# Performance work log

Measured on AMD Instinct MI355X. Metric: run time of the kernel, lower is better.

Reference implementation:

```python
import jax, jax.numpy as jnp
import numpy as np

DIM = 192


def _conv1x1(x, w, b):
    # x: [B, C_in, H, W], w: [C_out, C_in], b: [C_out]
    return jnp.einsum('bchw,oc->bohw', x, w) + b[None, :, None, None]


def setup_inputs() -> dict:
    key = jax.random.key(0)
    ks = jax.random.split(key, 7)
    B, T, C, H, W = 4, 16, DIM, 56, 56
    scale = 1.0 / np.sqrt(2 * C)
    return {
        'video': jax.random.normal(ks[0], (B, T, C, H, W), dtype=jnp.float32),
        'w_z': jax.random.normal(ks[1], (C, 2 * C), dtype=jnp.float32) * scale,
        'b_z': jax.random.normal(ks[2], (C,), dtype=jnp.float32) * scale,
        'w_r': jax.random.normal(ks[3], (C, 2 * C), dtype=jnp.float32) * scale,
        'b_r': jax.random.normal(ks[4], (C,), dtype=jnp.float32) * scale,
        'w_h': jax.random.normal(ks[5], (C, 2 * C), dtype=jnp.float32) * scale,
        'b_h': jax.random.normal(ks[6], (C,), dtype=jnp.float32) * scale,
    }


def reference(video, w_z, b_z, w_r, b_r, w_h, b_h):
    # video: [B, T, C, H, W]
    h0 = jnp.zeros_like(video[:, 0])  # [B, C, H, W]

    def step(h, x):
        xh = jnp.concatenate([x, h], axis=1)  # [B, 2C, H, W]
        z = jax.nn.sigmoid(_conv1x1(xh, w_z, b_z))
        r = jax.nn.sigmoid(_conv1x1(xh, w_r, b_r))
        xrh = jnp.concatenate([x, r * h], axis=1)
        h_new = (1.0 - z) * h + z * jnp.tanh(_conv1x1(xrh, w_h, b_h))
        return h_new, h_new

    # scan over time axis
    _, out = jax.lax.scan(step, h0, jnp.moveaxis(video, 1, 0))
    return jnp.moveaxis(out, 0, 1)  # [B, T, C, H, W]
```

## Files before the change

kernel.cpp:

```cpp
#include <hip/hip_runtime.h>
#include <cstdint>
#include <cstddef>

typedef _Float16 f16;
typedef _Float16 half8 __attribute__((ext_vector_type(8)));
typedef _Float16 half4 __attribute__((ext_vector_type(4)));
typedef float f32x4 __attribute__((ext_vector_type(4)));
typedef unsigned int u32;
typedef u32 u32x4 __attribute__((ext_vector_type(4)));

constexpr int CDIM = 192, HW = 3136, NBAT = 4, TSTEPS = 16;
constexpr int MTOT = NBAT * HW;
constexpr int NSUB = MTOT / 16;

constexpr size_t OFF_WX = 0;
constexpr size_t SZ_WX  = (size_t)6*36*64*8*2;
constexpr size_t OFF_WHB = OFF_WX + SZ_WX;
constexpr size_t SZ_WHB  = (size_t)12*3*6*64*8*2;
constexpr size_t OFF_U  = OFF_WHB + SZ_WHB;
constexpr size_t SZ_U   = (size_t)16*NSUB*12*3*64*4*2;
constexpr size_t NEED   = OFF_U + SZ_U;

constexpr size_t FB_WZR = 0;
constexpr size_t FB_SZ_WZR = (size_t)384*384*2;
constexpr size_t FB_WH  = FB_WZR + FB_SZ_WZR;


__global__ void pack_w(const float* __restrict__ wz, const float* __restrict__ wr,
                       const float* __restrict__ wh, char* __restrict__ ws) {
    int idx = blockIdx.x * 256 + threadIdx.x;
    if (idx >= 221184) return;
    f16* dst;
    int lane, i, k, c, gate;
    if (idx < 110592) {
        i = idx & 7; lane = (idx >> 3) & 63;
        int ktnt = idx >> 9, kt = ktnt / 36, nt = ktnt % 36;
        int n576 = nt * 16 + (lane & 15);
        gate = n576 / 192; c = n576 % 192;
        k = kt * 32 + (lane >> 4) * 8 + i;
        dst = (f16*)(ws + OFF_WX) + idx;
    } else {
        int j = idx - 110592;
        i = j & 7; lane = (j >> 3) & 63;
        int a = j >> 9, kt = a % 6, b = a / 6;
        gate = b % 3; int nsl = b / 3;
        c = nsl * 16 + (lane & 15);
        k = 192 + kt * 32 + (lane >> 4) * 8 + i;
        dst = (f16*)(ws + OFF_WHB) + j;
    }
    const float* W = (gate == 0) ? wz : (gate == 1) ? wr : wh;
    *dst = (f16)W[c * 384 + k];
}

__global__ __launch_bounds__(512, 2) void xproj(
    const float* __restrict__ video, char* __restrict__ ws,
    const float* __restrict__ bz, const float* __restrict__ br,
    const float* __restrict__ bh) {
    __shared__ __align__(16) char AX[2][24576];
    const f16* WX = (const f16*)(ws + OFF_WX);
    f16* U = (f16*)(ws + OFF_U);
    const int tid = threadIdx.x, w = tid >> 6, lane = tid & 63;
    const int l15 = lane & 15, lg = lane >> 4;
    const int mt = blockIdx.x;
    const int bb = mt / 49, hw0 = (mt % 49) * 64;
    const int t0 = blockIdx.y * 2;
    const int mg = w >> 2, nw = w & 3;
    const int swsh = (lane & 7) << 4;
    const int slot = (l15 & 7) << 4;

#pragma unroll
    for (int p = 0; p < 2; ++p) {
        const float* vs = video + ((size_t)(bb * TSTEPS + t0 + p) * CDIM) * HW + hw0 + lane;
#pragma unroll
        for (int g = 0; g < 3; ++g) {
            half8 hv;
#pragma unroll
            for (int j = 0; j < 8; ++j)
                hv[j] = (f16)__builtin_nontemporal_load(vs + (size_t)(w * 24 + g * 8 + j) * HW);
            *(half8*)(AX[p] + lane * 384 + ((w * 48 + g * 16) ^ swsh)) = hv;
        }
    }
    float vb[9];
#pragma unroll
    for (int r = 0; r < 9; ++r) {
        int n576 = nw * 144 + r * 16 + l15;
        int gate = n576 / 192, c = n576 % 192;
        vb[r] = (gate == 0 ? bz : (gate == 1 ? br : bh))[c];
    }
    __syncthreads();

    f32x4 acc[4][9];
#pragma unroll
    for (int i = 0; i < 4; ++i)
#pragma unroll
        for (int r = 0; r < 9; ++r)
#pragma unroll
            for (int q = 0; q < 4; ++q) acc[i][r][q] = vb[r];

#pragma unroll
    for (int kt = 0; kt < 6; ++kt) {
        half8 a[4];
#pragma unroll
        for (int i = 0; i < 4; ++i)
            a[i] = *(const half8*)(AX[mg] + (i * 16 + l15) * 384 + ((kt * 64 + lg * 16) ^ slot));
#pragma unroll
        for (int r = 0; r < 9; ++r) {
            half8 bf = *(const half8*)(WX + ((size_t)(kt * 36 + nw * 9 + r) * 64 + lane) * 8);
#pragma unroll
            for (int i = 0; i < 4; ++i)
                acc[i][r] = __builtin_amdgcn_mfma_f32_16x16x32_f16(a[i], bf, acc[i][r], 0, 0, 0);
        }
    }
    const int t = t0 + mg;
#pragma unroll
    for (int r = 0; r < 9; ++r) {
        int nb = nw * 9 + r;
        int gate = nb / 12, nsl = nb % 12;
#pragma unroll
        for (int i = 0; i < 4; ++i) {
            half4 hq;
#pragma unroll
            for (int q = 0; q < 4; ++q) hq[q] = (f16)acc[i][r][q];
            int sub = mt * 4 + i;
            f16* up = U + (((size_t)t * NSUB + sub) * 36 + (size_t)nsl * 3 + gate) * 256
                        + (size_t)lane * 4;
            *(half4*)up = hq;
        }
    }
}

__global__ __launch_bounds__(768, 3) void recur(const char* __restrict__ ws,
                                                float* __restrict__ dout) {
    __shared__ __align__(16) char AH[6144], RH[6144];
    const f16* WHB = (const f16*)(ws + OFF_WHB);
    const f16* U = (const f16*)(ws + OFF_U);
    const int tid = threadIdx.x, wv = tid >> 6, lane = tid & 63;
    const int l15 = lane & 15, lg = lane >> 4;
    const int sub = blockIdx.x;
    const int bb = sub / 196, hw0 = (sub % 196) * 16;
    const int slot = (l15 & 7) << 4;
    const int col = wv * 16 + l15;

    half8 wz_[6], wr_[6], wh_[6];
    {
        const f16* base = WHB + (size_t)wv * 9216 + lane * 8;
#pragma unroll
        for (int kt = 0; kt < 6; ++kt) {
            wz_[kt] = *(const half8*)(base + (0 * 6 + kt) * 512);
            wr_[kt] = *(const half8*)(base + (1 * 6 + kt) * 512);
            wh_[kt] = *(const half8*)(base + (2 * 6 + kt) * 512);
        }
    }
    *(uint64_t*)(AH + tid * 8) = 0ull;
    __syncthreads();

    const f16* ub = U + ((size_t)sub * 36 + (size_t)wv * 3) * 256 + (size_t)lane * 4;
    constexpr size_t UT = (size_t)NSUB * 36 * 256;
    half4 uz = *(const half4*)(ub);
    half4 ur = *(const half4*)(ub + 256);
    half4 uh = *(const half4*)(ub + 512);

    float h_own[4] = {0.f, 0.f, 0.f, 0.f};
    const int cb = (2 * col);
    float* ob = dout + ((size_t)(bb * TSTEPS) * CDIM + col) * HW + hw0 + lg * 4;

#pragma unroll 1
    for (int t = 0; t < TSTEPS; ++t) {
        f32x4 az = {0.f, 0.f, 0.f, 0.f}, ar = {0.f, 0.f, 0.f, 0.f};
#pragma unroll
        for (int kt = 0; kt < 6; ++kt) {
            half8 a0 = *(const half8*)(AH + l15 * 384 + ((kt * 64 + lg * 16) ^ slot));
            az = __builtin_amdgcn_mfma_f32_16x16x32_f16(a0, wz_[kt], az, 0, 0, 0);
            ar = __builtin_amdgcn_mfma_f32_16x16x32_f16(a0, wr_[kt], ar, 0, 0, 0);
        }
        float zg[4], ho[4];
#pragma unroll
        for (int q = 0; q < 4; ++q) {
            int row = lg * 4 + q;
            int b = cb ^ ((row & 7) << 4);
            float z = 1.f / (1.f + __expf(-(az[q] + (float)uz[q])));
            float r = 1.f / (1.f + __expf(-(ar[q] + (float)ur[q])));
            zg[q] = z; ho[q] = (1.f - z) * h_own[q];
            *(f16*)(RH + row * 384 + b) = (f16)(r * h_own[q]);
        }
        __syncthreads();

        half4 nz = uz, nr = ur, nh = uh;
        if (t + 1 < TSTEPS) {
            const f16* un = ub + (size_t)(t + 1) * UT;
            nz = *(const half4*)(un);
            nr = *(const half4*)(un + 256);
            nh = *(const half4*)(un + 512);
        }

        f32x4 ah = {0.f, 0.f, 0.f, 0.f};
#pragma unroll
        for (int kt = 0; kt < 6; ++kt) {
            half8 a0 = *(const half8*)(RH + l15 * 384 + ((kt * 64 + lg * 16) ^ slot));
            ah = __builtin_amdgcn_mfma_f32_16x16x32_f16(a0, wh_[kt], ah, 0, 0, 0);
        }
        f32x4 hv;
#pragma unroll
        for (int q = 0; q < 4; ++q) {
            int row = lg * 4 + q;
            int b = cb ^ ((row & 7) << 4);
            float e = __expf(2.f * (ah[q] + (float)uh[q]));
            float th = 1.f - 2.f / (e + 1.f);
            float hn = ho[q] + zg[q] * th;
            h_own[q] = hn; hv[q] = hn;
            *(f16*)(AH + row * 384 + b) = (f16)hn;
        }
        __builtin_nontemporal_store(hv, (f32x4*)(ob + (size_t)t * CDIM * HW));
        __syncthreads();
        uz = nz; ur = nr; uh = nh;
    }
}


__global__ void pack5(const float* __restrict__ wz, const float* __restrict__ wr,
                      const float* __restrict__ wh, char* __restrict__ ws) {
    int idx = blockIdx.x * 256 + threadIdx.x;
    const int ZRT = 384 * 384;
    int n, k, NT;
    float w;
    f16* dst;
    if (idx < ZRT) {
        n = idx / 384; k = idx - n * 384;
        w = (n < 192) ? wz[n * 384 + k] : wr[(n - 192) * 384 + k];
        dst = (f16*)(ws + FB_WZR); NT = 24;
    } else {
        int j = idx - ZRT;
        if (j >= 192 * 384) return;
        n = j / 384; k = j - n * 384;
        w = wh[n * 384 + k];
        dst = (f16*)(ws + FB_WH); NT = 12;
    }
    int kt = k >> 5, g = (k >> 3) & 3, i = k & 7, nt = n >> 4;
    int lane = (g << 4) | (n & 15);
    dst[((size_t)(kt * NT + nt) * 64 + lane) * 8 + i] = (f16)w;
}

__global__ __launch_bounds__(256, 2) void gru_fb(
    const float* __restrict__ video,
    const f16* __restrict__ wZR, const f16* __restrict__ wH,
    const float* __restrict__ bz, const float* __restrict__ br,
    const float* __restrict__ bh, float* __restrict__ dout) {
    __shared__ __align__(16) char smem[73728];
    char* AX = smem;
    char* AH = smem + 24576;
    char* RH = smem + 49152;
    const int tid = threadIdx.x, w = tid >> 6, lane = tid & 63;
    const int l15 = lane & 15, lg = lane >> 4;
    const int mt = blockIdx.x, bb = mt / 49, hw0 = (mt % 49) * 64;
    const int slot = (l15 & 7) << 4;
    const int swsh = (lane & 7) << 4;
    const float* vbase = video + (size_t)bb * TSTEPS * CDIM * HW + hw0 + lane;
    float* obase = dout + (size_t)bb * TSTEPS * CDIM * HW + hw0 + lane;
    float vbz[3], vbr[3], vbh[3];
#pragma unroll
    for (int r = 0; r < 3; ++r) {
        int c = w * 48 + r * 16 + l15;
        vbz[r] = bz[c]; vbr[r] = br[c]; vbh[r] = bh[c];
    }
    {
        half8 zz = {};
#pragma unroll
        for (int i = 0; i < 6; ++i) *(half8*)(AH + tid * 96 + i * 16) = zz;
#pragma unroll
        for (int g = 0; g < 6; ++g) {
            half8 hv;
#pragma unroll
            for (int j = 0; j < 8; ++j)
                hv[j] = (f16)__builtin_nontemporal_load(vbase + (size_t)(w * 48 + g * 8 + j) * HW);
            *(half8*)(AX + lane * 384 + ((w * 96 + g * 16) ^ swsh)) = hv;
        }
    }
    __syncthreads();
#pragma unroll 1
    for (int t = 0; t < TSTEPS; ++t) {
        f32x4 az[4][3], ar[4][3];
#pragma unroll
        for (int i = 0; i < 4; ++i)
#pragma unroll
            for (int r = 0; r < 3; ++r)
#pragma unroll
                for (int q = 0; q < 4; ++q) { az[i][r][q] = 0.f; ar[i][r][q] = 0.f; }
#pragma unroll
        for (int kt = 0; kt < 12; ++kt) {
            const char* ab = (kt < 6) ? AX : AH;
            int kb = (kt % 6) * 64 + lg * 16;
            half8 a[4];
#pragma unroll
            for (int i = 0; i < 4; ++i)
                a[i] = *(const half8*)(ab + (i * 16 + l15) * 384 + (kb ^ slot));
#pragma unroll
            for (int r = 0; r < 3; ++r) {
                half8 bzf = *(const half8*)(wZR + ((size_t)(kt * 24 + w * 3 + r) * 64 + lane) * 8);
                half8 brf = *(const half8*)(wZR + ((size_t)(kt * 24 + 12 + w * 3 + r) * 64 + lane) * 8);
#pragma unroll
                for (int i = 0; i < 4; ++i)
                    az[i][r] = __builtin_amdgcn_mfma_f32_16x16x32_f16(a[i], bzf, az[i][r], 0, 0, 0);
#pragma unroll
                for (int i = 0; i < 4; ++i)
                    ar[i][r] = __builtin_amdgcn_mfma_f32_16x16x32_f16(a[i], brf, ar[i][r], 0, 0, 0);
            }
        }
        float xn[6][8];
        if (t + 1 < TSTEPS) {
            const float* vs = vbase + (size_t)(t + 1) * CDIM * HW;
#pragma unroll
            for (int g = 0; g < 6; ++g)
#pragma unroll
                for (int j = 0; j < 8; ++j)
                    xn[g][j] = __builtin_nontemporal_load(vs + (size_t)(w * 48 + g * 8 + j) * HW);
        }
#pragma unroll
        for (int i = 0; i < 4; ++i)
#pragma unroll
            for (int r = 0; r < 3; ++r)
#pragma unroll
                for (int q = 0; q < 4; ++q) {
                    int row = i * 16 + lg * 4 + q;
                    int cb2 = 2 * (w * 48 + r * 16 + l15), sw = (row & 7) << 4;
                    float rg = 1.f / (1.f + __expf(-(ar[i][r][q] + vbr[r])));
                    float hvv = (float)*(const f16*)(AH + row * 384 + (cb2 ^ sw));
                    *(f16*)(RH + row * 384 + (cb2 ^ sw)) = (f16)(rg * hvv);
                }
        __syncthreads();
        f32x4 ac[4][3];
#pragma unroll
        for (int i = 0; i < 4; ++i)
#pragma unroll
            for (int r = 0; r < 3; ++r)
#pragma unroll
                for (int q = 0; q < 4; ++q) ac[i][r][q] = 0.f;
#pragma unroll
        for (int kt = 0; kt < 12; ++kt) {
            const char* ab = (kt < 6) ? AX : RH;
            int kb = (kt % 6) * 64 + lg * 16;
            half8 a[4];
#pragma unroll
            for (int i = 0; i < 4; ++i)
                a[i] = *(const half8*)(ab + (i * 16 + l15) * 384 + (kb ^ slot));
#pragma unroll
            for (int r = 0; r < 3; ++r) {
                half8 bf = *(const half8*)(wH + ((size_t)(kt * 12 + w * 3 + r) * 64 + lane) * 8);
#pragma unroll
                for (int i = 0; i < 4; ++i)
                    ac[i][r] = __builtin_amdgcn_mfma_f32_16x16x32_f16(a[i], bf, ac[i][r], 0, 0, 0);
            }
        }
#pragma unroll
        for (int i = 0; i < 4; ++i)
#pragma unroll
            for (int r = 0; r < 3; ++r)
#pragma unroll
                for (int q = 0; q < 4; ++q) {
                    int row = i * 16 + lg * 4 + q;
                    int cb2 = 2 * (w * 48 + r * 16 + l15), sw = (row & 7) << 4;
                    float zgv = 1.f / (1.f + __expf(-(az[i][r][q] + vbz[r])));
                    float e = __expf(2.f * (ac[i][r][q] + vbh[r]));
                    float th = 1.f - 2.f / (e + 1.f);
                    float hold = (float)*(const f16*)(AH + row * 384 + (cb2 ^ sw));
                    *(f16*)(AH + row * 384 + (cb2 ^ sw)) = (f16)((1.f - zgv) * hold + zgv * th);
                }
        __syncthreads();
        {
            float* ob = obase + (size_t)t * CDIM * HW;
#pragma unroll
            for (int g = 0; g < 6; ++g) {
                half8 hv = *(const half8*)(AH + lane * 384 + ((w * 96 + g * 16) ^ swsh));
#pragma unroll
                for (int j = 0; j < 8; ++j)
                    __builtin_nontemporal_store((float)hv[j], ob + (size_t)(w * 48 + g * 8 + j) * HW);
            }
            if (t + 1 < TSTEPS) {
#pragma unroll
                for (int g = 0; g < 6; ++g) {
                    half8 o;
#pragma unroll
                    for (int j = 0; j < 8; ++j) o[j] = (f16)xn[g][j];
                    *(half8*)(AX + lane * 384 + ((w * 96 + g * 16) ^ swsh)) = o;
                }
            }
        }
        __syncthreads();
    }
}

extern "C" void kernel_launch(void* const* d_in, const int* in_sizes, int n_in,
                              void* d_out, int out_size, void* d_ws, size_t ws_size,
                              hipStream_t stream) {
    const float* video = (const float*)d_in[0];
    const float* wz = (const float*)d_in[1];
    const float* bz = (const float*)d_in[2];
    const float* wr = (const float*)d_in[3];
    const float* br = (const float*)d_in[4];
    const float* wh = (const float*)d_in[5];
    const float* bh = (const float*)d_in[6];
    char* ws = (char*)d_ws;
    float* dout = (float*)d_out;

    if (ws_size >= NEED) {
        pack_w<<<864, 256, 0, stream>>>(wz, wr, wh, ws);
        xproj<<<dim3(196, 8), 512, 0, stream>>>(video, ws, bz, br, bh);
        recur<<<NSUB, 768, 0, stream>>>(ws, dout);
    } else {
        pack5<<<864, 256, 0, stream>>>(wz, wr, wh, ws);
        gru_fb<<<196, 256, 0, stream>>>(video, (const f16*)(ws + FB_WZR),
                                        (const f16*)(ws + FB_WH), bz, br, bh, dout);
    }
}
```

Measured before the change: 252.7 us.

## Interleave two pixel tiles per block in GRU recurrence to overlap dependent phases

Each recurrence block now processes two 16-pixel subtiles with staggered software pipelining, so one tile's gate MFMAs overlap the other tile's elementwise and LDS phases. The goal is to hide the latency of the serial MFMA → activation → barrier chain and to reuse the register-resident weights across twice as many pixels. This halves the grid and doubles LDS per block, which may reduce occupancy and leave fewer blocks to fill the GPU. The U writes in xproj also become nontemporal stores.

```diff
diff --git a/kernel.cpp b/kernel.cpp
--- a/kernel.cpp
+++ b/kernel.cpp
@@ -12,6 +12,7 @@
 constexpr int CDIM = 192, HW = 3136, NBAT = 4, TSTEPS = 16;
 constexpr int MTOT = NBAT * HW;
 constexpr int NSUB = MTOT / 16;
+constexpr int NCH  = MTOT / 32;
 
 constexpr size_t OFF_WX = 0;
 constexpr size_t SZ_WX  = (size_t)6*36*64*8*2;
@@ -124,20 +125,20 @@
             int sub = mt * 4 + i;
             f16* up = U + (((size_t)t * NSUB + sub) * 36 + (size_t)nsl * 3 + gate) * 256
                         + (size_t)lane * 4;
-            *(half4*)up = hq;
+            __builtin_nontemporal_store(hq, (half4*)up);
         }
     }
 }
 
 __global__ __launch_bounds__(768, 3) void recur(const char* __restrict__ ws,
                                                 float* __restrict__ dout) {
-    __shared__ __align__(16) char AH[6144], RH[6144];
+    __shared__ __align__(16) char AH0[6144], RH0[6144], AH1[6144], RH1[6144];
     const f16* WHB = (const f16*)(ws + OFF_WHB);
     const f16* U = (const f16*)(ws + OFF_U);
     const int tid = threadIdx.x, wv = tid >> 6, lane = tid & 63;
     const int l15 = lane & 15, lg = lane >> 4;
-    const int sub = blockIdx.x;
-    const int bb = sub / 196, hw0 = (sub % 196) * 16;
+    const int ch = blockIdx.x;
+    const int bb = ch / 98, hw0 = (ch % 98) * 32;
     const int slot = (l15 & 7) << 4;
     const int col = wv * 16 + l15;
 
@@ -151,68 +152,131 @@
             wh_[kt] = *(const half8*)(base + (2 * 6 + kt) * 512);
         }
     }
-    *(uint64_t*)(AH + tid * 8) = 0ull;
+    *(uint64_t*)(AH0 + tid * 8) = 0ull;
+    *(uint64_t*)(AH1 + tid * 8) = 0ull;
     __syncthreads();
 
-    const f16* ub = U + ((size_t)sub * 36 + (size_t)wv * 3) * 256 + (size_t)lane * 4;
+    int aoff[6];
+#pragma unroll
+    for (int kt = 0; kt < 6; ++kt) aoff[kt] = l15 * 384 + ((kt * 64 + lg * 16) ^ slot);
+    int coff[4];
+#pragma unroll
+    for (int q = 0; q < 4; ++q) {
+        int row = lg * 4 + q;
+        coff[q] = row * 384 + ((2 * col) ^ ((row & 7) << 4));
+    }
+
+    const f16* ub = U + ((size_t)(ch * 2) * 36 + (size_t)wv * 3) * 256 + (size_t)lane * 4;
     constexpr size_t UT = (size_t)NSUB * 36 * 256;
-    half4 uz = *(const half4*)(ub);
-    half4 ur = *(const half4*)(ub + 256);
-    half4 uh = *(const half4*)(ub + 512);
-
-    float h_own[4] = {0.f, 0.f, 0.f, 0.f};
-    const int cb = (2 * col);
-    float* ob = dout + ((size_t)(bb * TSTEPS) * CDIM + col) * HW + hw0 + lg * 4;
+    half4 uz0 = *(const half4*)(ub);
+    half4 ur0 = *(const half4*)(ub + 256);
+    half4 uh0 = *(const half4*)(ub + 512);
+    half4 uz1 = *(const half4*)(ub + 36 * 256);
+    half4 ur1 = *(const half4*)(ub + 36 * 256 + 256);
+    half4 uh1 = *(const half4*)(ub + 36 * 256 + 512);
+    half4 uh1p;
+
+    float h0_[4] = {0.f, 0.f, 0.f, 0.f}, h1_[4] = {0.f, 0.f, 0.f, 0.f};
+    float zg0[4], ho0[4], zg1[4], ho1[4];
+    f32x4 ah1;
+
+    float* ob0 = dout + ((size_t)(bb * TSTEPS) * CDIM + col) * HW + hw0 + lg * 4;
+    float* ob1 = ob0 + 16;
 
 #pragma unroll 1
     for (int t = 0; t < TSTEPS; ++t) {
-        f32x4 az = {0.f, 0.f, 0.f, 0.f}, ar = {0.f, 0.f, 0.f, 0.f};
+        f32x4 az0 = {0.f, 0.f, 0.f, 0.f}, ar0 = {0.f, 0.f, 0.f, 0.f};
 #pragma unroll
         for (int kt = 0; kt < 6; ++kt) {
-            half8 a0 = *(const half8*)(AH + l15 * 384 + ((kt * 64 + lg * 16) ^ slot));
-            az = __builtin_amdgcn_mfma_f32_16x16x32_f16(a0, wz_[kt], az, 0, 0, 0);
-            ar = __builtin_amdgcn_mfma_f32_16x16x32_f16(a0, wr_[kt], ar, 0, 0, 0);
-        }
-        float zg[4], ho[4];
+            half8 a = *(const half8*)(AH0 + aoff[kt]);
+            az0 = __builtin_amdgcn_mfma_f32_16x16x32_f16(a, wz_[kt], az0, 0, 0, 0);
+            ar0 = __builtin_amdgcn_mfma_f32_16x16x32_f16(a, wr_[kt], ar0, 0, 0, 0);
+        }
+        if (t > 0) {
+            f32x4 hv;
+#pragma unroll
+            for (int q = 0; q < 4; ++q) {
+                float e = __expf(2.f * (ah1[q] + (float)uh1p[q]));
+                float th = 1.f - 2.f / (e + 1.f);
+                float hn = ho1[q] + zg1[q] * th;
+                h1_[q] = hn; hv[q] = hn;
+                *(f16*)(AH1 + coff[q]) = (f16)hn;
+            }
+            __builtin_nontemporal_store(hv, (f32x4*)(ob1 + (size_t)(t - 1) * CDIM * HW));
+        }
+        __syncthreads();
+
+        f32x4 az1 = {0.f, 0.f, 0.f, 0.f}, ar1 = {0.f, 0.f, 0.f, 0.f};
+#pragma unroll
+        for (int kt = 0; kt < 6; ++kt) {
+            half8 a = *(const half8*)(AH1 + aoff[kt]);
+            az1 = __builtin_amdgcn_mfma_f32_16x16x32_f16(a, wz_[kt], az1, 0, 0, 0);
+            ar1 = __builtin_amdgcn_mfma_f32_16x16x32_f16(a, wr_[kt], ar1, 0, 0, 0);
+        }
 #pragma unroll
         for (int q = 0; q < 4; ++q) {
-            int row = lg * 4 + q;
-            int b = cb ^ ((row & 7) << 4);
-            float z = 1.f / (1.f + __expf(-(az[q] + (float)uz[q])));
-            float r = 1.f / (1.f + __expf(-(ar[q] + (float)ur[q])));
-            zg[q] = z; ho[q] = (1.f - z) * h_own[q];
-            *(f16*)(RH + row * 384 + b) = (f16)(r * h_own[q]);
-        }
-        __syncthreads();
-
-        half4 nz = uz, nr = ur, nh = uh;
+            float z = 1.f / (1.f + __expf(-(az0[q] + (float)uz0[q])));
+            float r = 1.f / (1.f + __expf(-(ar0[q] + (float)ur0[q])));
+            zg0[q] = z; ho0[q] = (1.f - z) * h0_[q];
+            *(f16*)(RH0 + coff[q]) = (f16)(r * h0_[q]);
+        }
+        __syncthreads();
+
+        f32x4 ah0 = {0.f, 0.f, 0.f, 0.f};
+#pragma unroll
+        for (int kt = 0; kt < 6; ++kt) {
+            half8 a = *(const half8*)(RH0 + aoff[kt]);
+            ah0 = __builtin_amdgcn_mfma_f32_16x16x32_f16(a, wh_[kt], ah0, 0, 0, 0);
+        }
+#pragma unroll
+        for (int q = 0; q < 4; ++q) {
+            float z = 1.f / (1.f + __expf(-(az1[q] + (float)uz1[q])));
+            float r = 1.f / (1.f + __expf(-(ar1[q] + (float)ur1[q])));
+            zg1[q] = z; ho1[q] = (1.f - z) * h1_[q];
+            *(f16*)(RH1 + coff[q]) = (f16)(r * h1_[q]);
+        }
         if (t + 1 < TSTEPS) {
             const f16* un = ub + (size_t)(t + 1) * UT;
-            nz = *(const half4*)(un);
-            nr = *(const half4*)(un + 256);
-            nh = *(const half4*)(un + 512);
-        }
-
-        f32x4 ah = {0.f, 0.f, 0.f, 0.f};
+            uz1 = *(const half4*)(un + 36 * 256);
+            ur1 = *(const half4*)(un + 36 * 256 + 256);
+        }
+        __syncthreads();
+
+        ah1[0] = 0.f; ah1[1] = 0.f; ah1[2] = 0.f; ah1[3] = 0.f;
 #pragma unroll
         for (int kt = 0; kt < 6; ++kt) {
-            half8 a0 = *(const half8*)(RH + l15 * 384 + ((kt * 64 + lg * 16) ^ slot));
-            ah = __builtin_amdgcn_mfma_f32_16x16x32_f16(a0, wh_[kt], ah, 0, 0, 0);
-        }
+            half8 a = *(const half8*)(RH1 + aoff[kt]);
+            ah1 = __builtin_amdgcn_mfma_f32_16x16x32_f16(a, wh_[kt], ah1, 0, 0, 0);
+        }
+        f32x4 hv0;
+#pragma unroll
+        for (int q = 0; q < 4; ++q) {
+            float e = __expf(2.f * (ah0[q] + (float)uh0[q]));
+            float th = 1.f - 2.f / (e + 1.f);
+            float hn = ho0[q] + zg0[q] * th;
+            h0_[q] = hn; hv0[q] = hn;
+            *(f16*)(AH0 + coff[q]) = (f16)hn;
+        }
+        __builtin_nontemporal_store(hv0, (f32x4*)(ob0 + (size_t)t * CDIM * HW));
+        uh1p = uh1;
+        if (t + 1 < TSTEPS) {
+            const f16* un = ub + (size_t)(t + 1) * UT;
+            uz0 = *(const half4*)(un);
+            ur0 = *(const half4*)(un + 256);
+            uh0 = *(const half4*)(un + 512);
+            uh1 = *(const half4*)(un + 36 * 256 + 512);
+        }
+        __syncthreads();
+    }
+    {
         f32x4 hv;
 #pragma unroll
         for (int q = 0; q < 4; ++q) {
-            int row = lg * 4 + q;
-            int b = cb ^ ((row & 7) << 4);
-            float e = __expf(2.f * (ah[q] + (float)uh[q]));
+            float e = __expf(2.f * (ah1[q] + (float)uh1p[q]));
             float th = 1.f - 2.f / (e + 1.f);
-            float hn = ho[q] + zg[q] * th;
-            h_own[q] = hn; hv[q] = hn;
-            *(f16*)(AH + row * 384 + b) = (f16)hn;
-        }
-        __builtin_nontemporal_store(hv, (f32x4*)(ob + (size_t)t * CDIM * HW));
-        __syncthreads();
-        uz = nz; ur = nr; uh = nh;
+            hv[q] = ho1[q] + zg1[q] * th;
+        }
+        __builtin_nontemporal_store(hv, (f32x4*)(ob1 + (size_t)15 * CDIM * HW));
     }
 }
 
@@ -404,7 +468,7 @@
     if (ws_size >= NEED) {
         pack_w<<<864, 256, 0, stream>>>(wz, wr, wh, ws);
         xproj<<<dim3(196, 8), 512, 0, stream>>>(video, ws, bz, br, bh);
-        recur<<<NSUB, 768, 0, stream>>>(ws, dout);
+        recur<<<NCH, 768, 0, stream>>>(ws, dout);
     } else {
         pack5<<<864, 256, 0, stream>>>(wz, wr, wh, ws);
         gru_fb<<<196, 256, 0, stream>>>(video, (const f16*)(ws + FB_WZR),
```

Measured after the change: 243.7 us. 1.04x faster.
